# Kernel tuning notes

Measured on AMD Instinct MI355X. Metric: run time of the kernel, lower is better.

## Reference

```python
import jax, jax.numpy as jnp
import numpy as np

PAD_H, PAD_W = 13, 17  # padded grid
GRID_H, GRID_W = 11, 15  # real hex grid (165 hexes)


def _build_convinds() -> np.ndarray:
    """Flat indices into the (13*17,) padded grid of the 7 hex neighbors per cell."""
    off0 = np.array([-17, -16, -1, 0, 1, 17, 18])
    off1 = np.array([-18, -17, -1, 0, 1, 16, 17])
    inds = np.zeros((GRID_H, GRID_W, 7), dtype=np.int32)
    for y in range(1, GRID_H + 1):
        for x in range(1, GRID_W + 1):
            base = y * PAD_W + x
            inds[y - 1, x - 1] = (off0 if y % 2 == 0 else off1) + base
    return inds.reshape(-1)  # (165*7,)


def setup_inputs() -> dict:
    key = jax.random.key(0)
    k1, k2, k3 = jax.random.split(key, 3)
    B, HEXDIM, OUT = 2048, 64, 64
    x = jax.random.normal(k1, (B, 165, HEXDIM), dtype=jnp.float32)
    W = jax.random.normal(k2, (OUT, 7 * HEXDIM), dtype=jnp.float32) * 0.05
    bias = jax.random.normal(k3, (OUT,), dtype=jnp.float32) * 0.05
    return {"x": x, "W": W, "bias": bias}


def reference(x, W, bias):
    convinds = jnp.asarray(_build_convinds())  # static (1155,)
    b, _, hexdim = x.shape
    xg = x.reshape(b, GRID_H, GRID_W, hexdim)
    padded = jnp.zeros((b, PAD_H, PAD_W, hexdim), dtype=x.dtype)
    padded = padded.at[:, 1:GRID_H + 1, 1:GRID_W + 1, :].set(xg)
    padded = padded.reshape(b, PAD_H * PAD_W, hexdim)
    # gather 7 neighbors per hex -> (b, 165, 7*hexdim)
    fc_in = padded[:, convinds, :].reshape(b, 165, 7 * hexdim)
    return jnp.einsum('bnk,ok->bno', fc_in, W) + bias
```

## Files before the change

### kernel.cpp

```cpp
#include <hip/hip_runtime.h>
#include <stdint.h>

typedef __bf16 bf16x8 __attribute__((ext_vector_type(8)));
typedef float floatx4 __attribute__((ext_vector_type(4)));
typedef uint32_t uint32x4 __attribute__((ext_vector_type(4)));

#define GRID_W   15
#define PAD_W    17
#define CELLS    221
#define HEXDIM   64
#define NHEX     165
#define OUTC     64
#define KDIM     448
#define LSTRIDE  72
#define LWORDS   (LSTRIDE/2)

__device__ __forceinline__ uint32_t pack2bf(float a, float b) {
    union { float f; uint32_t u; } ua, ub;
    ua.f = a; ub.f = b;
    uint32_t ra = (ua.u + 0x7fffu + ((ua.u >> 16) & 1u)) >> 16;
    uint32_t rb = (ub.u + 0x7fffu + ((ub.u >> 16) & 1u)) >> 16;
    return ra | (rb << 16);
}

__global__ __launch_bounds__(256, 2)
void hexconv_kernel(const float* __restrict__ x,
                    const float* __restrict__ W,
                    const float* __restrict__ bias,
                    float* __restrict__ out)
{
    __shared__ __align__(16) uint32_t sx[CELLS * LWORDS];

    const int tid  = threadIdx.x;
    const int b    = blockIdx.x;
    const int wave = tid >> 6;
    const int lane = tid & 63;
    const int col  = lane & 15;
    const int kq   = lane >> 4;

    const int o = wave * 16 + col;
    uint32x4 bw[14];
    {
        const float* wrow = W + (size_t)o * KDIM + kq * 8;
        #pragma unroll
        for (int ks = 0; ks < 14; ++ks) {
            float4 v0 = *(const float4*)(wrow + ks * 32);
            float4 v1 = *(const float4*)(wrow + ks * 32 + 4);
            uint32x4 t;
            t[0] = pack2bf(v0.x, v0.y);
            t[1] = pack2bf(v0.z, v0.w);
            t[2] = pack2bf(v1.x, v1.y);
            t[3] = pack2bf(v1.z, v1.w);
            bw[ks] = t;
        }
    }
    const float bias_o = bias[o];

    for (int i = tid; i < CELLS * LWORDS; i += 256) sx[i] = 0u;
    __syncthreads();

    {
        const float4* xs = (const float4*)(x + (size_t)b * NHEX * HEXDIM);
        for (int i = tid; i < NHEX * HEXDIM / 4; i += 256) {
            int n = i >> 4;
            int d = i & 15;
            float4 v = xs[i];
            int y0 = n / GRID_W, x0 = n - y0 * GRID_W;
            int cell = (y0 + 1) * PAD_W + (x0 + 1);
            uint32_t* dst = sx + cell * LWORDS + d * 2;
            uint2 p; p.x = pack2bf(v.x, v.y); p.y = pack2bf(v.z, v.w);
            *(uint2*)dst = p;
        }
    }
    __syncthreads();

    float* outb = out + (size_t)b * NHEX * OUTC;

    #pragma unroll 1
    for (int mt = 0; mt < 11; ++mt) {
        int n = mt * 16 + col;
        bool valid = (n < NHEX);
        int nn = valid ? n : 0;
        int y0 = nn / GRID_W, x0 = nn - y0 * GRID_W;
        int base = (y0 + 1) * PAD_W + (x0 + 1);
        bool use0 = (y0 & 1);

        const int off0[7] = {-17, -16, -1, 0, 1, 17, 18};
        const int off1[7] = {-18, -17, -1, 0, 1, 16, 17};
        int addr[7];
        #pragma unroll
        for (int j = 0; j < 7; ++j) {
            int cell = valid ? (base + (use0 ? off0[j] : off1[j])) : 16;
            addr[j] = cell * LWORDS + kq * 4;
        }

        floatx4 acc = {0.f, 0.f, 0.f, 0.f};
        #pragma unroll
        for (int ks = 0; ks < 14; ++ks) {
            int a_off = addr[ks >> 1] + (ks & 1) * 16;
            uint32x4 av = *(const uint32x4*)(sx + a_off);
            acc = __builtin_amdgcn_mfma_f32_16x16x32_bf16(
                      __builtin_bit_cast(bf16x8, av),
                      __builtin_bit_cast(bf16x8, bw[ks]),
                      acc, 0, 0, 0);
        }

        #pragma unroll
        for (int r = 0; r < 4; ++r) {
            int nr = mt * 16 + kq * 4 + r;
            if (nr < NHEX) outb[(size_t)nr * OUTC + o] = acc[r] + bias_o;
        }
    }
}

extern "C" void kernel_launch(void* const* d_in, const int* in_sizes, int n_in,
                              void* d_out, int out_size, void* d_ws, size_t ws_size,
                              hipStream_t stream) {
    const float* x    = (const float*)d_in[0];
    const float* W    = (const float*)d_in[1];
    const float* bias = (const float*)d_in[2];
    float* out        = (float*)d_out;

    int B = in_sizes[0] / (NHEX * HEXDIM);
    hexconv_kernel<<<B, 256, 0, stream>>>(x, W, bias, out);
}
```

Baseline: 203.3 us.

## Reuse A fragments across two output tiles and swizzle LDS layout

```diff
diff --git a/kernel.cpp b/kernel.cpp
--- a/kernel.cpp
+++ b/kernel.cpp
@@ -12,8 +12,7 @@
 #define NHEX     165
 #define OUTC     64
 #define KDIM     448
-#define LSTRIDE  72
-#define LWORDS   (LSTRIDE/2)
+#define CWORDS   32
 
 __device__ __forceinline__ uint32_t pack2bf(float a, float b) {
     union { float f; uint32_t u; } ua, ub;
@@ -29,7 +28,7 @@
                     const float* __restrict__ bias,
                     float* __restrict__ out)
 {
-    __shared__ __align__(16) uint32_t sx[CELLS * LWORDS];
+    __shared__ __align__(16) uint32_t sx[CELLS * CWORDS];
 
     const int tid  = threadIdx.x;
     const int b    = blockIdx.x;
@@ -37,10 +36,14 @@
     const int lane = tid & 63;
     const int col  = lane & 15;
     const int kq   = lane >> 4;
+    const int ow   = wave & 1;
+    const int mw   = wave >> 1;
 
-    const int o = wave * 16 + col;
-    uint32x4 bw[14];
-    {
+    uint32x4 bw[2][14];
+    float bias_o[2];
+    #pragma unroll
+    for (int ot = 0; ot < 2; ++ot) {
+        const int o = ow * 32 + ot * 16 + col;
         const float* wrow = W + (size_t)o * KDIM + kq * 8;
         #pragma unroll
         for (int ks = 0; ks < 14; ++ks) {
@@ -51,12 +54,12 @@
             t[1] = pack2bf(v0.z, v0.w);
             t[2] = pack2bf(v1.x, v1.y);
             t[3] = pack2bf(v1.z, v1.w);
-            bw[ks] = t;
+            bw[ot][ks] = t;
         }
+        bias_o[ot] = bias[o];
     }
-    const float bias_o = bias[o];
 
-    for (int i = tid; i < CELLS * LWORDS; i += 256) sx[i] = 0u;
+    for (int i = tid; i < CELLS * CWORDS; i += 256) sx[i] = 0u;
     __syncthreads();
 
     {
@@ -67,7 +70,8 @@
             float4 v = xs[i];
             int y0 = n / GRID_W, x0 = n - y0 * GRID_W;
             int cell = (y0 + 1) * PAD_W + (x0 + 1);
-            uint32_t* dst = sx + cell * LWORDS + d * 2;
+            int pc   = (d >> 1) ^ (cell & 7);
+            uint32_t* dst = sx + cell * CWORDS + pc * 4 + (d & 1) * 2;
             uint2 p; p.x = pack2bf(v.x, v.y); p.y = pack2bf(v.z, v.w);
             *(uint2*)dst = p;
         }
@@ -77,7 +81,7 @@
     float* outb = out + (size_t)b * NHEX * OUTC;
 
     #pragma unroll 1
-    for (int mt = 0; mt < 11; ++mt) {
+    for (int mt = mw; mt < 11; mt += 2) {
         int n = mt * 16 + col;
         bool valid = (n < NHEX);
         int nn = valid ? n : 0;
@@ -87,28 +91,36 @@
 
         const int off0[7] = {-17, -16, -1, 0, 1, 17, 18};
         const int off1[7] = {-18, -17, -1, 0, 1, 16, 17};
-        int addr[7];
+        int cbase[7], csw[7];
         #pragma unroll
         for (int j = 0; j < 7; ++j) {
             int cell = valid ? (base + (use0 ? off0[j] : off1[j])) : 16;
-            addr[j] = cell * LWORDS + kq * 4;
+            cbase[j] = cell * CWORDS;
+            csw[j]   = cell & 7;
         }
 
-        floatx4 acc = {0.f, 0.f, 0.f, 0.f};
+        floatx4 acc0 = {0.f, 0.f, 0.f, 0.f};
+        floatx4 acc1 = {0.f, 0.f, 0.f, 0.f};
         #pragma unroll
         for (int ks = 0; ks < 14; ++ks) {
-            int a_off = addr[ks >> 1] + (ks & 1) * 16;
-            uint32x4 av = *(const uint32x4*)(sx + a_off);
-            acc = __builtin_amdgcn_mfma_f32_16x16x32_bf16(
-                      __builtin_bit_cast(bf16x8, av),
-                      __builtin_bit_cast(bf16x8, bw[ks]),
-                      acc, 0, 0, 0);
+            int j = ks >> 1;
+            int chunk = ((ks & 1) * 4 + kq) ^ csw[j];
+            uint32x4 av = *(const uint32x4*)(sx + cbase[j] + chunk * 4);
+            bf16x8 a = __builtin_bit_cast(bf16x8, av);
+            acc0 = __builtin_amdgcn_mfma_f32_16x16x32_bf16(
+                       a, __builtin_bit_cast(bf16x8, bw[0][ks]), acc0, 0, 0, 0);
+            acc1 = __builtin_amdgcn_mfma_f32_16x16x32_bf16(
+                       a, __builtin_bit_cast(bf16x8, bw[1][ks]), acc1, 0, 0, 0);
         }
 
         #pragma unroll
         for (int r = 0; r < 4; ++r) {
             int nr = mt * 16 + kq * 4 + r;
-            if (nr < NHEX) outb[(size_t)nr * OUTC + o] = acc[r] + bias_o;
+            if (nr < NHEX) {
+                float* po = outb + (size_t)nr * OUTC + ow * 32 + col;
+                po[0]  = acc0[r] + bias_o[0];
+                po[16] = acc1[r] + bias_o[1];
+            }
         }
     }
 }
```

After: 210.9 us. +3.8%, slower.

## Split K across wave pairs, 2x2 register tiles, swizzled LDS, pre-converted bf16 weights

Applied to the files above, without the earlier changes.

```diff
diff --git a/kernel.cpp b/kernel.cpp
--- a/kernel.cpp
+++ b/kernel.cpp
@@ -12,8 +12,8 @@
 #define NHEX     165
 #define OUTC     64
 #define KDIM     448
-#define LSTRIDE  72
-#define LWORDS   (LSTRIDE/2)
+#define CWORDS   32
+#define SXWORDS  (CELLS * CWORDS)
 
 __device__ __forceinline__ uint32_t pack2bf(float a, float b) {
     union { float f; uint32_t u; } ua, ub;
@@ -23,13 +23,72 @@
     return ra | (rb << 16);
 }
 
-__global__ __launch_bounds__(256, 2)
+__global__ void wprep_kernel(const float* __restrict__ W, uint32_t* __restrict__ Wbf) {
+    int i = blockIdx.x * 256 + threadIdx.x;
+    float4 v = ((const float4*)W)[i];
+    uint2 p; p.x = pack2bf(v.x, v.y); p.y = pack2bf(v.z, v.w);
+    ((uint2*)Wbf)[i] = p;
+}
+
+__device__ __forceinline__ floatx4 mfma16(bf16x8 a, uint32x4 b, floatx4 c) {
+    return __builtin_amdgcn_mfma_f32_16x16x32_bf16(a, __builtin_bit_cast(bf16x8, b), c, 0, 0, 0);
+}
+
+template<int KH>
+__device__ __forceinline__ void pair_accs(const uint32_t* __restrict__ sx,
+                                          int mtA, int mtB, int col, int kq,
+                                          const uint32x4 bw[2][7],
+                                          floatx4& a00, floatx4& a01,
+                                          floatx4& a10, floatx4& a11)
+{
+    const int off0[7] = {-17, -16, -1, 0, 1, 17, 18};
+    const int off1[7] = {-18, -17, -1, 0, 1, 16, 17};
+
+    int cellA[4], cellB[4];
+    #pragma unroll
+    for (int two = 0; two < 2; ++two) {
+        int mt = two ? mtB : mtA;
+        int* cells = two ? cellB : cellA;
+        int n = mt * 16 + col;
+        bool valid = (n < NHEX);
+        int nn = valid ? n : 0;
+        int y0 = nn / GRID_W, x0 = nn - y0 * GRID_W;
+        int base = (y0 + 1) * PAD_W + (x0 + 1);
+        bool use0 = (y0 & 1);
+        #pragma unroll
+        for (int jj = 0; jj < 4; ++jj) {
+            const int j = KH * 3 + jj;
+            cells[jj] = valid ? (base + (use0 ? off0[j] : off1[j])) : 16;
+        }
+    }
+
+    #pragma unroll
+    for (int ksl = 0; ksl < 7; ++ksl) {
+        const int ks = KH * 7 + ksl;
+        const int jj = (ks >> 1) - KH * 3;
+        const int h  = ks & 1;
+        int cA = cellA[jj], cB = cellB[jj];
+        int chA = ((h * 4 + kq) ^ (cA & 7));
+        int chB = ((h * 4 + kq) ^ (cB & 7));
+        uint32x4 avA = *(const uint32x4*)(sx + cA * CWORDS + chA * 4);
+        uint32x4 avB = *(const uint32x4*)(sx + cB * CWORDS + chB * 4);
+        bf16x8 aA = __builtin_bit_cast(bf16x8, avA);
+        bf16x8 aB = __builtin_bit_cast(bf16x8, avB);
+        a00 = mfma16(aA, bw[0][ksl], a00);
+        a10 = mfma16(aB, bw[0][ksl], a10);
+        a01 = mfma16(aA, bw[1][ksl], a01);
+        a11 = mfma16(aB, bw[1][ksl], a11);
+    }
+}
+
+__global__ __launch_bounds__(512, 4)
 void hexconv_kernel(const float* __restrict__ x,
-                    const float* __restrict__ W,
+                    const uint32_t* __restrict__ Wbf,
                     const float* __restrict__ bias,
                     float* __restrict__ out)
 {
-    __shared__ __align__(16) uint32_t sx[CELLS * LWORDS];
+    __shared__ __align__(16) uint32_t sx[SXWORDS];
+    __shared__ __align__(16) floatx4 red[2][4][4][64];
 
     const int tid  = threadIdx.x;
     const int b    = blockIdx.x;
@@ -37,37 +96,35 @@
     const int lane = tid & 63;
     const int col  = lane & 15;
     const int kq   = lane >> 4;
+    const int kh   = wave & 1;
+    const int ow   = (wave >> 1) & 1;
+    const int mw   = wave >> 2;
 
-    const int o = wave * 16 + col;
-    uint32x4 bw[14];
-    {
-        const float* wrow = W + (size_t)o * KDIM + kq * 8;
+    uint32x4 bw[2][7];
+    #pragma unroll
+    for (int ot = 0; ot < 2; ++ot) {
+        int o = ow * 32 + ot * 16 + col;
+        const uint32_t* wp = Wbf + o * (KDIM / 2) + kh * 112 + kq * 4;
         #pragma unroll
-        for (int ks = 0; ks < 14; ++ks) {
-            float4 v0 = *(const float4*)(wrow + ks * 32);
-            float4 v1 = *(const float4*)(wrow + ks * 32 + 4);
-            uint32x4 t;
-            t[0] = pack2bf(v0.x, v0.y);
-            t[1] = pack2bf(v0.z, v0.w);
-            t[2] = pack2bf(v1.x, v1.y);
-            t[3] = pack2bf(v1.z, v1.w);
-            bw[ks] = t;
-        }
+        for (int ksl = 0; ksl < 7; ++ksl)
+            bw[ot][ksl] = *(const uint32x4*)(wp + ksl * 16);
     }
-    const float bias_o = bias[o];
+    const float b0 = bias[ow * 32 + col];
+    const float b1 = bias[ow * 32 + 16 + col];
 
-    for (int i = tid; i < CELLS * LWORDS; i += 256) sx[i] = 0u;
+    for (int i = tid; i < SXWORDS; i += 512) sx[i] = 0u;
     __syncthreads();
 
     {
         const float4* xs = (const float4*)(x + (size_t)b * NHEX * HEXDIM);
-        for (int i = tid; i < NHEX * HEXDIM / 4; i += 256) {
+        for (int i = tid; i < NHEX * HEXDIM / 4; i += 512) {
             int n = i >> 4;
             int d = i & 15;
             float4 v = xs[i];
             int y0 = n / GRID_W, x0 = n - y0 * GRID_W;
             int cell = (y0 + 1) * PAD_W + (x0 + 1);
-            uint32_t* dst = sx + cell * LWORDS + d * 2;
+            int pc   = (d >> 1) ^ (cell & 7);
+            uint32_t* dst = sx + cell * CWORDS + pc * 4 + (d & 1) * 2;
             uint2 p; p.x = pack2bf(v.x, v.y); p.y = pack2bf(v.z, v.w);
             *(uint2*)dst = p;
         }
@@ -75,40 +132,47 @@
     __syncthreads();
 
     float* outb = out + (size_t)b * NHEX * OUTC;
+    const int region = mw * 2 + ow;
 
     #pragma unroll 1
-    for (int mt = 0; mt < 11; ++mt) {
-        int n = mt * 16 + col;
-        bool valid = (n < NHEX);
-        int nn = valid ? n : 0;
-        int y0 = nn / GRID_W, x0 = nn - y0 * GRID_W;
-        int base = (y0 + 1) * PAD_W + (x0 + 1);
-        bool use0 = (y0 & 1);
+    for (int t = 0; t < 3; ++t) {
+        int mtA = mw + t * 4;
+        int mtB = mtA + 2;
 
-        const int off0[7] = {-17, -16, -1, 0, 1, 17, 18};
-        const int off1[7] = {-18, -17, -1, 0, 1, 16, 17};
-        int addr[7];
-        #pragma unroll
-        for (int j = 0; j < 7; ++j) {
-            int cell = valid ? (base + (use0 ? off0[j] : off1[j])) : 16;
-            addr[j] = cell * LWORDS + kq * 4;
+        floatx4 a00 = {0.f,0.f,0.f,0.f}, a01 = {0.f,0.f,0.f,0.f};
+        floatx4 a10 = {0.f,0.f,0.f,0.f}, a11 = {0.f,0.f,0.f,0.f};
+        if (kh == 0) pair_accs<0>(sx, mtA, mtB, col, kq, bw, a00, a01, a10, a11);
+        else         pair_accs<1>(sx, mtA, mtB, col, kq, bw, a00, a01, a10, a11);
+
+        int buf = t & 1;
+        if (kh) {
+            red[buf][region][0][lane] = a00;
+            red[buf][region][1][lane] = a01;
+            red[buf][region][2][lane] = a10;
+            red[buf][region][3][lane] = a11;
         }
-
-        floatx4 acc = {0.f, 0.f, 0.f, 0.f};
-        #pragma unroll
-        for (int ks = 0; ks < 14; ++ks) {
-            int a_off = addr[ks >> 1] + (ks & 1) * 16;
-            uint32x4 av = *(const uint32x4*)(sx + a_off);
-            acc = __builtin_amdgcn_mfma_f32_16x16x32_bf16(
-                      __builtin_bit_cast(bf16x8, av),
-                      __builtin_bit_cast(bf16x8, bw[ks]),
-                      acc, 0, 0, 0);
-        }
-
-        #pragma unroll
-        for (int r = 0; r < 4; ++r) {
-            int nr = mt * 16 + kq * 4 + r;
-            if (nr < NHEX) outb[(size_t)nr * OUTC + o] = acc[r] + bias_o;
+        __syncthreads();
+        if (!kh) {
+            floatx4 p0 = red[buf][region][0][lane];
+            floatx4 p1 = red[buf][region][1][lane];
+            floatx4 p2 = red[buf][region][2][lane];
+            floatx4 p3 = red[buf][region][3][lane];
+            a00 += p0; a01 += p1; a10 += p2; a11 += p3;
+            #pragma unroll
+            for (int rr = 0; rr < 4; ++rr) {
+                int nrA = mtA * 16 + kq * 4 + rr;
+                if (nrA < NHEX) {
+                    float* po = outb + (size_t)nrA * OUTC + ow * 32 + col;
+                    po[0]  = a00[rr] + b0;
+                    po[16] = a01[rr] + b1;
+                }
+                int nrB = mtB * 16 + kq * 4 + rr;
+                if (nrB < NHEX) {
+                    float* po = outb + (size_t)nrB * OUTC + ow * 32 + col;
+                    po[0]  = a10[rr] + b0;
+                    po[16] = a11[rr] + b1;
+                }
+            }
         }
     }
 }
@@ -120,7 +184,10 @@
     const float* W    = (const float*)d_in[1];
     const float* bias = (const float*)d_in[2];
     float* out        = (float*)d_out;
+    uint32_t* Wbf     = (uint32_t*)d_ws;
+
+    wprep_kernel<<<28, 256, 0, stream>>>(W, Wbf);
 
     int B = in_sizes[0] / (NHEX * HEXDIM);
-    hexconv_kernel<<<B, 256, 0, stream>>>(x, W, bias, out);
+    hexconv_kernel<<<B, 512, 0, stream>>>(x, Wbf, bias, out);
 }
```

New measurement: 181.5 us. -10.7%, faster.

## Batch samples per block with double-buffered LDS, 32x32 MFMA, prepacked bf16 weights

Applied to the files above, without the earlier changes.

```diff
diff --git a/kernel.cpp b/kernel.cpp
--- a/kernel.cpp
+++ b/kernel.cpp
@@ -2,18 +2,18 @@
 #include <stdint.h>
 
 typedef __bf16 bf16x8 __attribute__((ext_vector_type(8)));
-typedef float floatx4 __attribute__((ext_vector_type(4)));
+typedef float floatx16 __attribute__((ext_vector_type(16)));
 typedef uint32_t uint32x4 __attribute__((ext_vector_type(4)));
 
 #define GRID_W   15
 #define PAD_W    17
 #define CELLS    221
-#define HEXDIM   64
 #define NHEX     165
 #define OUTC     64
 #define KDIM     448
-#define LSTRIDE  72
-#define LWORDS   (LSTRIDE/2)
+#define CWORDS   32
+#define SXW      (CELLS * CWORDS)
+#define NSAMP    4
 
 __device__ __forceinline__ uint32_t pack2bf(float a, float b) {
     union { float f; uint32_t u; } ua, ub;
@@ -23,93 +23,124 @@
     return ra | (rb << 16);
 }
 
+__global__ void wprep_kernel(const float* __restrict__ W, uint32_t* __restrict__ Wbf) {
+    int i = blockIdx.x * 256 + threadIdx.x;
+    float4 v = ((const float4*)W)[i];
+    uint2 p; p.x = pack2bf(v.x, v.y); p.y = pack2bf(v.z, v.w);
+    ((uint2*)Wbf)[i] = p;
+}
+
 __global__ __launch_bounds__(256, 2)
 void hexconv_kernel(const float* __restrict__ x,
-                    const float* __restrict__ W,
+                    const uint32_t* __restrict__ Wbf,
                     const float* __restrict__ bias,
-                    float* __restrict__ out)
+                    float* __restrict__ out, int B)
 {
-    __shared__ __align__(16) uint32_t sx[CELLS * LWORDS];
+    __shared__ __align__(16) uint32_t sx[2][SXW];
 
     const int tid  = threadIdx.x;
-    const int b    = blockIdx.x;
+    const int lane = tid & 63;
     const int wave = tid >> 6;
-    const int lane = tid & 63;
-    const int col  = lane & 15;
-    const int kq   = lane >> 4;
+    const int ln31 = lane & 31;
+    const int h    = lane >> 5;
+    const int ow   = wave & 1;
+    const int mw   = wave >> 1;
 
-    const int o = wave * 16 + col;
-    uint32x4 bw[14];
+    const int o = ow * 32 + ln31;
+    uint32x4 bw[28];
     {
-        const float* wrow = W + (size_t)o * KDIM + kq * 8;
+        const uint32_t* wp = Wbf + o * (KDIM / 2) + h * 4;
         #pragma unroll
-        for (int ks = 0; ks < 14; ++ks) {
-            float4 v0 = *(const float4*)(wrow + ks * 32);
-            float4 v1 = *(const float4*)(wrow + ks * 32 + 4);
-            uint32x4 t;
-            t[0] = pack2bf(v0.x, v0.y);
-            t[1] = pack2bf(v0.z, v0.w);
-            t[2] = pack2bf(v1.x, v1.y);
-            t[3] = pack2bf(v1.z, v1.w);
-            bw[ks] = t;
-        }
+        for (int ks = 0; ks < 28; ++ks)
+            bw[ks] = *(const uint32x4*)(wp + ks * 8);
     }
     const float bias_o = bias[o];
 
-    for (int i = tid; i < CELLS * LWORDS; i += 256) sx[i] = 0u;
+    for (int i = tid; i < 2 * SXW / 4; i += 256)
+        ((uint32x4*)sx)[i] = (uint32x4){0u, 0u, 0u, 0u};
     __syncthreads();
 
-    {
-        const float4* xs = (const float4*)(x + (size_t)b * NHEX * HEXDIM);
-        for (int i = tid; i < NHEX * HEXDIM / 4; i += 256) {
-            int n = i >> 4;
-            int d = i & 15;
+    const int b0 = blockIdx.x * NSAMP;
+
+    auto stage = [&](int b, uint32_t* buf) {
+        const float4* xs = (const float4*)(x + (size_t)b * NHEX * 64);
+        #pragma unroll 1
+        for (int i = tid; i < NHEX * 16; i += 256) {
+            int n = i >> 4, d = i & 15;
             float4 v = xs[i];
             int y0 = n / GRID_W, x0 = n - y0 * GRID_W;
             int cell = (y0 + 1) * PAD_W + (x0 + 1);
-            uint32_t* dst = sx + cell * LWORDS + d * 2;
+            int pc   = (d >> 1) ^ (cell & 7);
             uint2 p; p.x = pack2bf(v.x, v.y); p.y = pack2bf(v.z, v.w);
-            *(uint2*)dst = p;
+            *(uint2*)(buf + cell * CWORDS + pc * 4 + (d & 1) * 2) = p;
         }
-    }
-    __syncthreads();
+    };
 
-    float* outb = out + (size_t)b * NHEX * OUTC;
-
-    #pragma unroll 1
-    for (int mt = 0; mt < 11; ++mt) {
-        int n = mt * 16 + col;
+    auto calc_cells = [&](int mt, int* cells) {
+        int n = mt * 32 + ln31;
         bool valid = (n < NHEX);
         int nn = valid ? n : 0;
         int y0 = nn / GRID_W, x0 = nn - y0 * GRID_W;
         int base = (y0 + 1) * PAD_W + (x0 + 1);
         bool use0 = (y0 & 1);
-
         const int off0[7] = {-17, -16, -1, 0, 1, 17, 18};
         const int off1[7] = {-18, -17, -1, 0, 1, 16, 17};
-        int addr[7];
         #pragma unroll
-        for (int j = 0; j < 7; ++j) {
-            int cell = valid ? (base + (use0 ? off0[j] : off1[j])) : 16;
-            addr[j] = cell * LWORDS + kq * 4;
+        for (int j = 0; j < 7; ++j)
+            cells[j] = valid ? (base + (use0 ? off0[j] : off1[j])) : 16;
+    };
+
+    if (b0 < B) stage(b0, sx[0]);
+    __syncthreads();
+
+    #pragma unroll 1
+    for (int s = 0; s < NSAMP; ++s) {
+        int b = b0 + s;
+        const uint32_t* cur = sx[s & 1];
+        if (s + 1 < NSAMP && b + 1 < B) stage(b + 1, sx[(s + 1) & 1]);
+
+        if (b < B) {
+            int cA[7], cB[7], cC[7];
+            calc_cells(mw,     cA);
+            calc_cells(mw + 2, cB);
+            calc_cells(mw + 4, cC);
+
+            floatx16 aA = {0,0,0,0,0,0,0,0,0,0,0,0,0,0,0,0};
+            floatx16 aB = {0,0,0,0,0,0,0,0,0,0,0,0,0,0,0,0};
+            floatx16 aC = {0,0,0,0,0,0,0,0,0,0,0,0,0,0,0,0};
+
+            #pragma unroll
+            for (int ks = 0; ks < 28; ++ks) {
+                const int j  = ks >> 2;
+                const int lc = (ks & 3) * 2 + h;
+                int eA = cA[j], eB = cB[j], eC = cC[j];
+                uint32x4 vA = *(const uint32x4*)(cur + eA * CWORDS + (lc ^ (eA & 7)) * 4);
+                uint32x4 vB = *(const uint32x4*)(cur + eB * CWORDS + (lc ^ (eB & 7)) * 4);
+                uint32x4 vC = *(const uint32x4*)(cur + eC * CWORDS + (lc ^ (eC & 7)) * 4);
+                aA = __builtin_amdgcn_mfma_f32_32x32x16_bf16(
+                         __builtin_bit_cast(bf16x8, vA),
+                         __builtin_bit_cast(bf16x8, bw[ks]), aA, 0, 0, 0);
+                aB = __builtin_amdgcn_mfma_f32_32x32x16_bf16(
+                         __builtin_bit_cast(bf16x8, vB),
+                         __builtin_bit_cast(bf16x8, bw[ks]), aB, 0, 0, 0);
+                aC = __builtin_amdgcn_mfma_f32_32x32x16_bf16(
+                         __builtin_bit_cast(bf16x8, vC),
+                         __builtin_bit_cast(bf16x8, bw[ks]), aC, 0, 0, 0);
+            }
+
+            float* outb = out + (size_t)b * NHEX * OUTC;
+            #pragma unroll
+            for (int r = 0; r < 16; ++r) {
+                int row = (r & 3) + 8 * (r >> 2) + 4 * h;
+                int nA = mw * 32 + row;
+                int nB = (mw + 2) * 32 + row;
+                int nC = (mw + 4) * 32 + row;
+                outb[(size_t)nA * OUTC + o] = aA[r] + bias_o;
+                outb[(size_t)nB * OUTC + o] = aB[r] + bias_o;
+                if (nC < NHEX) outb[(size_t)nC * OUTC + o] = aC[r] + bias_o;
+            }
         }
-
-        floatx4 acc = {0.f, 0.f, 0.f, 0.f};
-        #pragma unroll
-        for (int ks = 0; ks < 14; ++ks) {
-            int a_off = addr[ks >> 1] + (ks & 1) * 16;
-            uint32x4 av = *(const uint32x4*)(sx + a_off);
-            acc = __builtin_amdgcn_mfma_f32_16x16x32_bf16(
-                      __builtin_bit_cast(bf16x8, av),
-                      __builtin_bit_cast(bf16x8, bw[ks]),
-                      acc, 0, 0, 0);
-        }
-
-        #pragma unroll
-        for (int r = 0; r < 4; ++r) {
-            int nr = mt * 16 + kq * 4 + r;
-            if (nr < NHEX) outb[(size_t)nr * OUTC + o] = acc[r] + bias_o;
-        }
+        __syncthreads();
     }
 }
 
@@ -120,7 +151,11 @@
     const float* W    = (const float*)d_in[1];
     const float* bias = (const float*)d_in[2];
     float* out        = (float*)d_out;
+    uint32_t* Wbf     = (uint32_t*)d_ws;
 
-    int B = in_sizes[0] / (NHEX * HEXDIM);
-    hexconv_kernel<<<B, 256, 0, stream>>>(x, W, bias, out);
+    wprep_kernel<<<28, 256, 0, stream>>>(W, Wbf);
+
+    int B = in_sizes[0] / (NHEX * 64);
+    int grid = (B + NSAMP - 1) / NSAMP;
+    hexconv_kernel<<<grid, 256, 0, stream>>>(x, Wbf, bias, out, B);
 }
```

Measured after the change: 263.5 us. 1.3x slower.
